# Optimization experiments

Measured on AMD Instinct MI355X. Metric: run time of the kernel, lower is better.

Reference implementation:

```python
import jax, jax.numpy as jnp
import numpy as np

N_NODES = 50000
N_EDGES = 800000
F_IN, F_HID, F_OUT = 512, 64, 16


def setup_inputs() -> dict:
    key = jax.random.key(0)
    k1, k2, k3, k4, k5, k6 = jax.random.split(key, 6)
    x = jax.random.normal(k1, (N_NODES, F_IN), dtype=jnp.float32)
    edge_index = jax.random.randint(k2, (2, N_EDGES), 0, N_NODES, dtype=jnp.int64)
    # Glorot-style init for GCNConv linear weights, zero bias (PyG default)
    W1 = jax.random.normal(k3, (F_IN, F_HID), dtype=jnp.float32) * (1.0 / np.sqrt(F_IN))
    b1 = jnp.zeros((F_HID,), dtype=jnp.float32)
    W2 = jax.random.normal(k4, (F_HID, F_OUT), dtype=jnp.float32) * (1.0 / np.sqrt(F_HID))
    b2 = jnp.zeros((F_OUT,), dtype=jnp.float32)
    return {"x": x, "edge_index": edge_index, "W1": W1, "b1": b1, "W2": W2, "b2": b2}


def _gcn_conv(x, W, b, src, dst, norm, num_nodes):
    # x' = W x, then symmetric-normalized neighbor aggregation (scatter-add at dst)
    h = x @ W                                   # [N, F_out]
    msg = h[src] * norm[:, None]                # gather + scale  [E+N, F_out]
    out = jax.ops.segment_sum(msg, dst, num_segments=num_nodes)
    return out + b


def _gcn_norm(edge_index, num_nodes):
    # add self loops, compute deg^{-1/2}[src] * deg^{-1/2}[dst]
    loops = jnp.arange(num_nodes, dtype=edge_index.dtype)
    src = jnp.concatenate([edge_index[0], loops])
    dst = jnp.concatenate([edge_index[1], loops])
    deg = jax.ops.segment_sum(jnp.ones_like(dst, dtype=jnp.float32), dst,
                              num_segments=num_nodes)
    dinv = jnp.where(deg > 0, jax.lax.rsqrt(deg), 0.0)
    norm = dinv[src] * dinv[dst]                # [E+N]
    return src, dst, norm


def reference(x, edge_index, W1, b1, W2, b2):
    num_nodes = x.shape[0]
    src, dst, norm = _gcn_norm(edge_index, num_nodes)
    h = _gcn_conv(x, W1, b1, src, dst, norm, num_nodes)
    h = jax.nn.relu(h)
    return _gcn_conv(h, W2, b2, src, dst, norm, num_nodes)
```

## Files before the change

### kernel.cpp

```cpp
#include <hip/hip_runtime.h>

#define N_NODES 50000
#define N_EDGES 800000
#define F_IN    512
#define F_HID   64
#define F_OUT   16
#define NT      (N_NODES / 16)
#define GRID    512
#define CAP     64

typedef short bf16x8 __attribute__((ext_vector_type(8)));
typedef float f32x4  __attribute__((ext_vector_type(4)));

__device__ __forceinline__ short bhi_of(float v) {
    return (short)(__float_as_uint(v) >> 16);
}
__device__ __forceinline__ short blo_of(float v) {
    float hif = __uint_as_float(__float_as_uint(v) & 0xffff0000u);
    return (short)(__float_as_uint(v - hif) >> 16);
}

__global__ __launch_bounds__(256) void k_build(const int* __restrict__ src,
                                               const int* __restrict__ dst,
                                               int* __restrict__ count,
                                               int* __restrict__ padded) {
    int e = blockIdx.x * 256 + threadIdx.x;
    if (e < N_EDGES) {
        int d = dst[e];
        int pos = atomicAdd(&count[d], 1);
        if (pos < CAP) padded[(size_t)d * CAP + pos] = src[e];
    }
}

__global__ __launch_bounds__(512) void k_gemm1(const float* __restrict__ x,
                                               const float* __restrict__ W1,
                                               float* __restrict__ h) {
    __shared__ __align__(16) float Abuf[2][8192];
    __shared__ float red[2][4][16][17];
    const int wave = threadIdx.x >> 6;
    const int lane = threadIdx.x & 63;
    const int m  = lane & 15, q = lane >> 4;
    const int kw = wave >> 2;
    const int cg = wave & 3;

    bf16x8 Bh[8], Bl[8];
#pragma unroll
    for (int s = 0; s < 8; ++s)
#pragma unroll
        for (int j = 0; j < 8; ++j) {
            float w = W1[(size_t)((kw * 8 + s) * 32 + q * 8 + j) * F_HID + cg * 16 + m];
            Bh[s][j] = bhi_of(w);
            Bl[s][j] = blo_of(w);
        }

    const int t0 = (int)(((long)NT * blockIdx.x) / GRID);
    const int t1 = (int)(((long)NT * (blockIdx.x + 1)) / GRID);

    int tile = t0;
    {
        const char* gb = (const char*)(x + (size_t)tile * 16 * F_IN);
        char* lb = (char*)&Abuf[0][0];
#pragma unroll
        for (int i = 0; i < 4; ++i) {
            const int c = wave * 4 + i;
            const int o = c * 1024 + lane * 16;
            const int sw = ((c >> 1) & 7) << 4;
            *(f32x4*)(lb + (o ^ sw)) = *(const f32x4*)(gb + o);
        }
    }
    __syncthreads();

    int p = 0;
    const int swr = (m & 7) << 4;
    while (true) {
        const int next = tile + 1;

        f32x4 v[4];
        if (next < t1) {
            const char* gb = (const char*)(x + (size_t)next * 16 * F_IN);
#pragma unroll
            for (int i = 0; i < 4; ++i) {
                const int o = (wave * 4 + i) * 1024 + lane * 16;
                v[i] = *(const f32x4*)(gb + o);
            }
        }

        f32x4 accA = {0, 0, 0, 0}, accB = {0, 0, 0, 0};
        const char* ab = (const char*)&Abuf[p][0];
#pragma unroll
        for (int s = 0; s < 8; ++s) {
            const int abase = m * 2048 + kw * 1024 + s * 128 + q * 32;
            f32x4 x0 = *(const f32x4*)(ab + (abase ^ swr));
            f32x4 x1 = *(const f32x4*)(ab + ((abase + 16) ^ swr));
            bf16x8 ahi, alo;
#pragma unroll
            for (int j = 0; j < 4; ++j) {
                ahi[j] = bhi_of(x0[j]);  alo[j] = blo_of(x0[j]);
                ahi[j + 4] = bhi_of(x1[j]);  alo[j + 4] = blo_of(x1[j]);
            }
            if (s & 1) {
                accB = __builtin_amdgcn_mfma_f32_16x16x32_bf16(ahi, Bh[s], accB, 0, 0, 0);
                accB = __builtin_amdgcn_mfma_f32_16x16x32_bf16(alo, Bh[s], accB, 0, 0, 0);
                accB = __builtin_amdgcn_mfma_f32_16x16x32_bf16(ahi, Bl[s], accB, 0, 0, 0);
            } else {
                accA = __builtin_amdgcn_mfma_f32_16x16x32_bf16(ahi, Bh[s], accA, 0, 0, 0);
                accA = __builtin_amdgcn_mfma_f32_16x16x32_bf16(alo, Bh[s], accA, 0, 0, 0);
                accA = __builtin_amdgcn_mfma_f32_16x16x32_bf16(ahi, Bl[s], accA, 0, 0, 0);
            }
        }
        f32x4 acc = accA + accB;

        if (next < t1) {
            char* lb = (char*)&Abuf[p ^ 1][0];
#pragma unroll
            for (int i = 0; i < 4; ++i) {
                const int c = wave * 4 + i;
                const int o = c * 1024 + lane * 16;
                const int sw = ((c >> 1) & 7) << 4;
                *(f32x4*)(lb + (o ^ sw)) = v[i];
            }
        }

        if (kw == 1) {
#pragma unroll
            for (int r = 0; r < 4; ++r)
                red[p][cg][q * 4 + r][m] = acc[r];
        }
        __syncthreads();

        if (kw == 0) {
            const int r0 = tile * 16;
#pragma unroll
            for (int r = 0; r < 4; ++r)
                h[(size_t)(r0 + q * 4 + r) * F_HID + cg * 16 + m] =
                    acc[r] + red[p][cg][q * 4 + r][m];
        }
        if (next >= t1) break;
        tile = next;
        p ^= 1;
    }
}

__global__ __launch_bounds__(256) void k_agg64f(const int* __restrict__ count,
                                                const int* __restrict__ padded,
                                                const float* __restrict__ h,
                                                const float* __restrict__ b1,
                                                const float* __restrict__ W2,
                                                float* __restrict__ h2,
                                                float* __restrict__ dinv) {
    __shared__ float h1s[16][68];
    __shared__ float W2s[64][17];
    for (int i = threadIdx.x; i < 64 * 16; i += 256)
        W2s[i >> 4][i & 15] = W2[i];

    const int lane = threadIdx.x & 63;
    const int wv   = threadIdx.x >> 6;
    const int slot = lane >> 4;
    const int fl   = lane & 15;
    const int node = blockIdx.x * 16 + wv * 4 + slot;
    const int cnt  = min(count[node], CAP);
    const float dn = rsqrtf((float)cnt + 1.0f);
    if (fl == 0) dinv[node] = dn;
    const int* lst = padded + (size_t)node * CAP;

    f32x4 accA = (*(const f32x4*)&h[(size_t)node * F_HID + fl * 4]) * dn;
    f32x4 accB = {0, 0, 0, 0};
    int k = 0;
    for (; k + 4 <= cnt; k += 4) {
        int4 S = *(const int4*)(lst + k);
        float w0 = rsqrtf((float)count[S.x] + 1.0f);
        float w1 = rsqrtf((float)count[S.y] + 1.0f);
        float w2 = rsqrtf((float)count[S.z] + 1.0f);
        float w3 = rsqrtf((float)count[S.w] + 1.0f);
        f32x4 v0 = *(const f32x4*)&h[(size_t)S.x * F_HID + fl * 4];
        f32x4 v1 = *(const f32x4*)&h[(size_t)S.y * F_HID + fl * 4];
        f32x4 v2 = *(const f32x4*)&h[(size_t)S.z * F_HID + fl * 4];
        f32x4 v3 = *(const f32x4*)&h[(size_t)S.w * F_HID + fl * 4];
        accA += v0 * w0;
        accB += v1 * w1;
        accA += v2 * w2;
        accB += v3 * w3;
    }
    for (; k < cnt; ++k) {
        int s = lst[k];
        accA += (*(const f32x4*)&h[(size_t)s * F_HID + fl * 4])
              * rsqrtf((float)count[s] + 1.0f);
    }
    f32x4 r = (accA + accB) * dn;
    const f32x4 bb = *(const f32x4*)&b1[fl * 4];
    f32x4 h1v;
#pragma unroll
    for (int i = 0; i < 4; ++i)
        h1v[i] = fmaxf(r[i] + bb[i], 0.0f);
    *(f32x4*)&h1s[wv * 4 + slot][fl * 4] = h1v;
    __syncthreads();

    const int nd = threadIdx.x >> 4, o = threadIdx.x & 15;
    float s = 0.0f;
#pragma unroll
    for (int kk = 0; kk < 64; ++kk)
        s = fmaf(h1s[nd][kk], W2s[kk][o], s);
    h2[(size_t)(blockIdx.x * 16 + nd) * F_OUT + o] = s;
}

__global__ __launch_bounds__(256) void k_agg16(const int* __restrict__ count,
                                               const int* __restrict__ padded,
                                               const float* __restrict__ dinv,
                                               const float* __restrict__ h2,
                                               const float* __restrict__ b2,
                                               float* __restrict__ out) {
    const int lane = threadIdx.x & 63;
    const int wv   = threadIdx.x >> 6;
    const int slot = lane >> 2;
    const int fl   = lane & 3;
    const int node = blockIdx.x * 64 + wv * 16 + slot;
    if (node >= N_NODES) return;
    const int cnt  = min(count[node], CAP);
    const float dn = dinv[node];
    const int* lst = padded + (size_t)node * CAP;

    f32x4 accA = (*(const f32x4*)&h2[(size_t)node * F_OUT + fl * 4]) * dn;
    f32x4 accB = {0, 0, 0, 0};
    int k = 0;
    for (; k + 4 <= cnt; k += 4) {
        int4 S = *(const int4*)(lst + k);
        float w0 = dinv[S.x], w1 = dinv[S.y], w2 = dinv[S.z], w3 = dinv[S.w];
        f32x4 v0 = *(const f32x4*)&h2[(size_t)S.x * F_OUT + fl * 4];
        f32x4 v1 = *(const f32x4*)&h2[(size_t)S.y * F_OUT + fl * 4];
        f32x4 v2 = *(const f32x4*)&h2[(size_t)S.z * F_OUT + fl * 4];
        f32x4 v3 = *(const f32x4*)&h2[(size_t)S.w * F_OUT + fl * 4];
        accA += v0 * w0;
        accB += v1 * w1;
        accA += v2 * w2;
        accB += v3 * w3;
    }
    for (; k < cnt; ++k) {
        int s = lst[k];
        accA += (*(const f32x4*)&h2[(size_t)s * F_OUT + fl * 4]) * dinv[s];
    }
    f32x4 r = (accA + accB) * dn;
    const f32x4 bb = *(const f32x4*)&b2[fl * 4];
    *(f32x4*)&out[(size_t)node * F_OUT + fl * 4] = r + bb;
}

extern "C" void kernel_launch(void* const* d_in, const int* in_sizes, int n_in,
                              void* d_out, int out_size, void* d_ws, size_t ws_size,
                              hipStream_t stream) {
    const float* x  = (const float*)d_in[0];
    const int*   ei = (const int*)d_in[1];
    const float* W1 = (const float*)d_in[2];
    const float* b1 = (const float*)d_in[3];
    const float* W2 = (const float*)d_in[4];
    const float* b2 = (const float*)d_in[5];
    float* out = (float*)d_out;

    const int* src = ei;
    const int* dst = ei + N_EDGES;

    int* wsi = (int*)d_ws;
    int* count   = wsi;
    int* padded  = count + 50176;
    float* dinv  = (float*)(padded + (size_t)50176 * CAP);
    float* h     = dinv + 50176;
    float* h2    = h + (size_t)N_NODES * F_HID;

    (void)hipMemsetAsync(count, 0, 50176 * sizeof(int), stream);

    k_build<<<(N_EDGES + 255) / 256, 256, 0, stream>>>(src, dst, count, padded);
    k_gemm1<<<GRID, 512, 0, stream>>>(x, W1, h);

    k_agg64f<<<N_NODES / 16, 256, 0, stream>>>(count, padded, h, b1, W2, h2, dinv);
    k_agg16<<<(N_NODES + 63) / 64, 256, 0, stream>>>(count, padded, dinv, h2, b2, out);
}
```

Before: 266.7 us.

## Fuse edge-list build into GEMM kernel, precompute dinv, unroll gathers by eight

Merges the adjacency build into the first GEMM kernel. Even blocks do their share of edges before the GEMM and odd blocks after it, so the atomic scatter overlaps the memory-bound x streaming and one launch is removed. A small kernel now computes dinv once per node, so the aggregation no longer computes rsqrt on count at every neighbor. Both aggregation loops are unrolled to eight neighbors for more memory-level parallelism. The trade-off is one extra launch and possible contention between the atomics and the GEMM traffic.

```diff
diff --git a/kernel.cpp b/kernel.cpp
--- a/kernel.cpp
+++ b/kernel.cpp
@@ -20,21 +20,22 @@
     return (short)(__float_as_uint(v - hif) >> 16);
 }
 
-__global__ __launch_bounds__(256) void k_build(const int* __restrict__ src,
-                                               const int* __restrict__ dst,
-                                               int* __restrict__ count,
-                                               int* __restrict__ padded) {
-    int e = blockIdx.x * 256 + threadIdx.x;
-    if (e < N_EDGES) {
-        int d = dst[e];
-        int pos = atomicAdd(&count[d], 1);
-        if (pos < CAP) padded[(size_t)d * CAP + pos] = src[e];
-    }
-}
-
-__global__ __launch_bounds__(512) void k_gemm1(const float* __restrict__ x,
-                                               const float* __restrict__ W1,
-                                               float* __restrict__ h) {
+__global__ __launch_bounds__(512) void k_mega(const float* __restrict__ x,
+                                              const float* __restrict__ W1,
+                                              const int* __restrict__ src,
+                                              const int* __restrict__ dst,
+                                              int* __restrict__ count,
+                                              int* __restrict__ padded,
+                                              float* __restrict__ h) {
+    const bool buildFirst = (blockIdx.x & 1) == 0;
+    if (buildFirst) {
+        for (int e = blockIdx.x * 512 + threadIdx.x; e < N_EDGES; e += GRID * 512) {
+            int d = dst[e];
+            int pos = atomicAdd(&count[d], 1);
+            if (pos < CAP) padded[(size_t)d * CAP + pos] = src[e];
+        }
+    }
+
     __shared__ __align__(16) float Abuf[2][8192];
     __shared__ float red[2][4][16][17];
     const int wave = threadIdx.x >> 6;
@@ -139,15 +140,29 @@
         tile = next;
         p ^= 1;
     }
+
+    if (!buildFirst) {
+        for (int e = blockIdx.x * 512 + threadIdx.x; e < N_EDGES; e += GRID * 512) {
+            int d = dst[e];
+            int pos = atomicAdd(&count[d], 1);
+            if (pos < CAP) padded[(size_t)d * CAP + pos] = src[e];
+        }
+    }
+}
+
+__global__ __launch_bounds__(256) void k_dinv(const int* __restrict__ count,
+                                              float* __restrict__ dinv) {
+    int i = blockIdx.x * 256 + threadIdx.x;
+    if (i < N_NODES) dinv[i] = rsqrtf((float)count[i] + 1.0f);
 }
 
 __global__ __launch_bounds__(256) void k_agg64f(const int* __restrict__ count,
                                                 const int* __restrict__ padded,
+                                                const float* __restrict__ dinv,
                                                 const float* __restrict__ h,
                                                 const float* __restrict__ b1,
                                                 const float* __restrict__ W2,
-                                                float* __restrict__ h2,
-                                                float* __restrict__ dinv) {
+                                                float* __restrict__ h2) {
     __shared__ float h1s[16][68];
     __shared__ float W2s[64][17];
     for (int i = threadIdx.x; i < 64 * 16; i += 256)
@@ -159,19 +174,37 @@
     const int fl   = lane & 15;
     const int node = blockIdx.x * 16 + wv * 4 + slot;
     const int cnt  = min(count[node], CAP);
-    const float dn = rsqrtf((float)cnt + 1.0f);
-    if (fl == 0) dinv[node] = dn;
+    const float dn = dinv[node];
     const int* lst = padded + (size_t)node * CAP;
 
     f32x4 accA = (*(const f32x4*)&h[(size_t)node * F_HID + fl * 4]) * dn;
     f32x4 accB = {0, 0, 0, 0};
     int k = 0;
+    for (; k + 8 <= cnt; k += 8) {
+        int4 S0 = *(const int4*)(lst + k);
+        int4 S1 = *(const int4*)(lst + k + 4);
+        float w0 = dinv[S0.x], w1 = dinv[S0.y], w2 = dinv[S0.z], w3 = dinv[S0.w];
+        float w4 = dinv[S1.x], w5 = dinv[S1.y], w6 = dinv[S1.z], w7 = dinv[S1.w];
+        f32x4 v0 = *(const f32x4*)&h[(size_t)S0.x * F_HID + fl * 4];
+        f32x4 v1 = *(const f32x4*)&h[(size_t)S0.y * F_HID + fl * 4];
+        f32x4 v2 = *(const f32x4*)&h[(size_t)S0.z * F_HID + fl * 4];
+        f32x4 v3 = *(const f32x4*)&h[(size_t)S0.w * F_HID + fl * 4];
+        f32x4 v4 = *(const f32x4*)&h[(size_t)S1.x * F_HID + fl * 4];
+        f32x4 v5 = *(const f32x4*)&h[(size_t)S1.y * F_HID + fl * 4];
+        f32x4 v6 = *(const f32x4*)&h[(size_t)S1.z * F_HID + fl * 4];
+        f32x4 v7 = *(const f32x4*)&h[(size_t)S1.w * F_HID + fl * 4];
+        accA += v0 * w0;
+        accB += v1 * w1;
+        accA += v2 * w2;
+        accB += v3 * w3;
+        accA += v4 * w4;
+        accB += v5 * w5;
+        accA += v6 * w6;
+        accB += v7 * w7;
+    }
     for (; k + 4 <= cnt; k += 4) {
         int4 S = *(const int4*)(lst + k);
-        float w0 = rsqrtf((float)count[S.x] + 1.0f);
-        float w1 = rsqrtf((float)count[S.y] + 1.0f);
-        float w2 = rsqrtf((float)count[S.z] + 1.0f);
-        float w3 = rsqrtf((float)count[S.w] + 1.0f);
+        float w0 = dinv[S.x], w1 = dinv[S.y], w2 = dinv[S.z], w3 = dinv[S.w];
         f32x4 v0 = *(const f32x4*)&h[(size_t)S.x * F_HID + fl * 4];
         f32x4 v1 = *(const f32x4*)&h[(size_t)S.y * F_HID + fl * 4];
         f32x4 v2 = *(const f32x4*)&h[(size_t)S.z * F_HID + fl * 4];
@@ -183,8 +216,7 @@
     }
     for (; k < cnt; ++k) {
         int s = lst[k];
-        accA += (*(const f32x4*)&h[(size_t)s * F_HID + fl * 4])
-              * rsqrtf((float)count[s] + 1.0f);
+        accA += (*(const f32x4*)&h[(size_t)s * F_HID + fl * 4]) * dinv[s];
     }
     f32x4 r = (accA + accB) * dn;
     const f32x4 bb = *(const f32x4*)&b1[fl * 4];
@@ -222,6 +254,28 @@
     f32x4 accA = (*(const f32x4*)&h2[(size_t)node * F_OUT + fl * 4]) * dn;
     f32x4 accB = {0, 0, 0, 0};
     int k = 0;
+    for (; k + 8 <= cnt; k += 8) {
+        int4 S0 = *(const int4*)(lst + k);
+        int4 S1 = *(const int4*)(lst + k + 4);
+        float w0 = dinv[S0.x], w1 = dinv[S0.y], w2 = dinv[S0.z], w3 = dinv[S0.w];
+        float w4 = dinv[S1.x], w5 = dinv[S1.y], w6 = dinv[S1.z], w7 = dinv[S1.w];
+        f32x4 v0 = *(const f32x4*)&h2[(size_t)S0.x * F_OUT + fl * 4];
+        f32x4 v1 = *(const f32x4*)&h2[(size_t)S0.y * F_OUT + fl * 4];
+        f32x4 v2 = *(const f32x4*)&h2[(size_t)S0.z * F_OUT + fl * 4];
+        f32x4 v3 = *(const f32x4*)&h2[(size_t)S0.w * F_OUT + fl * 4];
+        f32x4 v4 = *(const f32x4*)&h2[(size_t)S1.x * F_OUT + fl * 4];
+        f32x4 v5 = *(const f32x4*)&h2[(size_t)S1.y * F_OUT + fl * 4];
+        f32x4 v6 = *(const f32x4*)&h2[(size_t)S1.z * F_OUT + fl * 4];
+        f32x4 v7 = *(const f32x4*)&h2[(size_t)S1.w * F_OUT + fl * 4];
+        accA += v0 * w0;
+        accB += v1 * w1;
+        accA += v2 * w2;
+        accB += v3 * w3;
+        accA += v4 * w4;
+        accB += v5 * w5;
+        accA += v6 * w6;
+        accB += v7 * w7;
+    }
     for (; k + 4 <= cnt; k += 4) {
         int4 S = *(const int4*)(lst + k);
         float w0 = dinv[S.x], w1 = dinv[S.y], w2 = dinv[S.z], w3 = dinv[S.w];
@@ -266,9 +320,9 @@
 
     (void)hipMemsetAsync(count, 0, 50176 * sizeof(int), stream);
 
-    k_build<<<(N_EDGES + 255) / 256, 256, 0, stream>>>(src, dst, count, padded);
-    k_gemm1<<<GRID, 512, 0, stream>>>(x, W1, h);
-
-    k_agg64f<<<N_NODES / 16, 256, 0, stream>>>(count, padded, h, b1, W2, h2, dinv);
+    k_mega<<<GRID, 512, 0, stream>>>(x, W1, src, dst, count, padded, h);
+    k_dinv<<<(N_NODES + 255) / 256, 256, 0, stream>>>(count, dinv);
+
+    k_agg64f<<<N_NODES / 16, 256, 0, stream>>>(count, padded, dinv, h, b1, W2, h2);
     k_agg16<<<(N_NODES + 63) / 64, 256, 0, stream>>>(count, padded, dinv, h2, b2, out);
 }
```

Result: faster. 243.3 us (-8.8%).
